# Kernel tuning notes

Measured on AMD Instinct MI355X. Metric: run time of the kernel, lower is better.

## Reference

```python
import jax, jax.numpy as jnp
import numpy as np

V = 32000   # vocab
T = 256     # context len
C = 384     # n_embed
H = 6       # heads
D = 64      # head dim (HEAD_SIZE // NUM_HEADS)
L = 6       # blocks
B = 16      # batch
FF = 4 * C


def setup_inputs() -> dict:
    key = jax.random.key(0)
    ks = jax.random.split(key, 16)
    s = 0.02
    p = {}
    p["x_ids"] = jax.random.randint(ks[0], (B, T), 0, V)
    p["y_ids"] = jax.random.randint(ks[1], (B, T), 0, V)
    p["tok_emb"] = jax.random.normal(ks[2], (V, C), jnp.float32) * s
    p["pos_emb"] = jax.random.normal(ks[3], (T, C), jnp.float32) * s
    p["Wq"] = jax.random.normal(ks[4], (L, H, C, D), jnp.float32) * s
    p["Wk"] = jax.random.normal(ks[5], (L, H, C, D), jnp.float32) * s
    p["Wv"] = jax.random.normal(ks[6], (L, H, C, D), jnp.float32) * s
    p["Wo"] = jax.random.normal(ks[7], (L, H * D, C), jnp.float32) * s
    p["bo"] = jnp.zeros((L, C), jnp.float32)
    p["ln1_s"] = jnp.ones((L, C), jnp.float32)
    p["ln1_b"] = jnp.zeros((L, C), jnp.float32)
    p["ln2_s"] = jnp.ones((L, C), jnp.float32)
    p["ln2_b"] = jnp.zeros((L, C), jnp.float32)
    p["W1"] = jax.random.normal(ks[8], (L, C, FF), jnp.float32) * s
    p["b1"] = jnp.zeros((L, FF), jnp.float32)
    p["W2"] = jax.random.normal(ks[9], (L, FF, C), jnp.float32) * s
    p["b2"] = jnp.zeros((L, C), jnp.float32)
    p["lnf_s"] = jnp.ones((C,), jnp.float32)
    p["lnf_b"] = jnp.zeros((C,), jnp.float32)
    p["Whead"] = jax.random.normal(ks[10], (C, V), jnp.float32) * s
    p["bhead"] = jnp.zeros((V,), jnp.float32)
    return p


def _ln(x, scale, bias, eps=1e-5):
    m = x.mean(-1, keepdims=True)
    v = ((x - m) ** 2).mean(-1, keepdims=True)
    return (x - m) * jax.lax.rsqrt(v + eps) * scale + bias


def reference(x_ids, y_ids, tok_emb, pos_emb, Wq, Wk, Wv, Wo, bo,
              ln1_s, ln1_b, ln2_s, ln2_b, W1, b1, W2, b2,
              lnf_s, lnf_b, Whead, bhead):
    Bq, Tq = x_ids.shape
    x = tok_emb[x_ids] + pos_emb[:Tq]                      # [B,T,C]
    mask = jnp.tril(jnp.ones((Tq, Tq), bool))
    scale = C ** -0.5  # NOTE: original scales by input dim C, not head dim
    for l in range(L):
        h = _ln(x, ln1_s[l], ln1_b[l])
        q = jnp.einsum('btc,hcd->bhtd', h, Wq[l])
        k = jnp.einsum('btc,hcd->bhtd', h, Wk[l])
        v = jnp.einsum('btc,hcd->bhtd', h, Wv[l])
        att = jnp.einsum('bhtd,bhsd->bhts', q, k) * scale
        att = jnp.where(mask, att, -jnp.inf)
        att = jax.nn.softmax(att, axis=-1)
        o = jnp.einsum('bhts,bhsd->bhtd', att, v)
        o = o.transpose(0, 2, 1, 3).reshape(Bq, Tq, H * D)  # concat heads
        x = x + o @ Wo[l] + bo[l]
        h2 = _ln(x, ln2_s[l], ln2_b[l])
        x = x + jax.nn.relu(h2 @ W1[l] + b1[l]) @ W2[l] + b2[l]
    x = _ln(x, lnf_s, lnf_b)
    logits = x @ Whead + bhead                             # [B,T,V]
    logp = jax.nn.log_softmax(logits, axis=-1)
    loss = -jnp.take_along_axis(logp, y_ids[..., None], axis=-1).mean()
    return (logits, loss)
```

## Files before the change

### kernel.cpp

```cpp
#include <hip/hip_runtime.h>

typedef unsigned short u16;
typedef u16   u16x8 __attribute__((ext_vector_type(8)));
typedef short s16x8 __attribute__((ext_vector_type(8)));
typedef float f32x4 __attribute__((ext_vector_type(4)));

#define NV 32000
#define NT 256
#define NC 384
#define NH 6
#define ND 64
#define NL 6
#define NB 16
#define NFF 1536
#define NM (NB*NT)
#define QKVSZ (NB*NH*NT*ND)
#define NSLAB (NV/128)

__device__ __forceinline__ u16 f2bf(float f){
    unsigned x = __builtin_bit_cast(unsigned, f);
    x += 0x7fffu + ((x>>16)&1u);
    return (u16)(x>>16);
}

__device__ __forceinline__ void gload_lds16(const u16* g, u16* l){
    __builtin_amdgcn_global_load_lds((const __attribute__((address_space(1))) unsigned int*)g,
                                     (__attribute__((address_space(3))) unsigned int*)l, 16, 0, 0);
}

__global__ __launch_bounds__(256) void embed_ln(const int* __restrict__ ids,
        const float* __restrict__ tok, const float* __restrict__ pos,
        const float* __restrict__ sc, const float* __restrict__ bi,
        float* __restrict__ x, u16* __restrict__ out){
    int row  = blockIdx.x*4 + (threadIdx.x>>6);
    int lane = threadIdx.x & 63;
    int t = row & (NT-1);
    const float* tr = tok + (size_t)ids[row]*NC;
    const float* pr = pos + (size_t)t*NC;
    float* xr = x + (size_t)row*NC;
    float v[6]; float sum = 0.f, sq = 0.f;
    #pragma unroll
    for (int i=0;i<6;++i){
        int c = lane+64*i;
        v[i] = tr[c] + pr[c];
        xr[c] = v[i];
        sum += v[i]; sq += v[i]*v[i];
    }
    #pragma unroll
    for (int off=1; off<64; off<<=1){ sum += __shfl_xor(sum,off); sq += __shfl_xor(sq,off); }
    float mean = sum*(1.f/NC);
    float rstd = rsqrtf(sq*(1.f/NC) - mean*mean + 1e-5f);
    u16* orow = out + (size_t)row*NC;
    #pragma unroll
    for (int i=0;i<6;++i){ int c = lane+64*i; orow[c] = f2bf((v[i]-mean)*rstd*sc[c] + bi[c]); }
}

__global__ __launch_bounds__(256) void ln_kernel(const float* __restrict__ x,
        const float* __restrict__ sc, const float* __restrict__ bi, u16* __restrict__ out){
    int row  = blockIdx.x*4 + (threadIdx.x>>6);
    int lane = threadIdx.x & 63;
    const float* xr = x + (size_t)row*NC;
    float v[6]; float sum = 0.f, sq = 0.f;
    #pragma unroll
    for (int i=0;i<6;++i){ v[i]=xr[lane+64*i]; sum+=v[i]; sq+=v[i]*v[i]; }
    #pragma unroll
    for (int off=1; off<64; off<<=1){ sum += __shfl_xor(sum,off); sq += __shfl_xor(sq,off); }
    float mean = sum*(1.f/NC);
    float rstd = rsqrtf(sq*(1.f/NC) - mean*mean + 1e-5f);
    u16* orow = out + (size_t)row*NC;
    #pragma unroll
    for (int i=0;i<6;++i){ int c = lane+64*i; orow[c] = f2bf((v[i]-mean)*rstd*sc[c] + bi[c]); }
}

struct TDesc {
    const float* in; u16* out;
    int Cc; int nx; int perZ; int obDiv; int oStride; int start;
    long inBatch; long oS1; long oS2; float scale;
};
struct TPack { TDesc d[7]; };

__global__ __launch_bounds__(256) void tconv_all(TPack p){
    __shared__ float tile[32][33];
    int bid = blockIdx.x;
    int e = 0;
    #pragma unroll
    for (int i=1;i<7;++i) e += (bid >= p.d[i].start) ? 1 : 0;
    TDesc D = p.d[e];
    int local = bid - D.start;
    int bz  = local / D.perZ; int rem = local - bz*D.perZ;
    int cy  = rem / D.nx;     int cx  = rem - cy*D.nx;
    int r0 = cy*32, c0 = cx*32;
    const float* ib = D.in + (size_t)bz*D.inBatch;
    u16* ob = D.out + (size_t)(bz/D.obDiv)*D.oS1 + (size_t)(bz%D.obDiv)*D.oS2;
    int tx = threadIdx.x & 31, ty = threadIdx.x >> 5;
    #pragma unroll
    for (int i=0;i<4;++i) tile[ty+8*i][tx] = ib[(size_t)(r0+ty+8*i)*D.Cc + (c0+tx)];
    __syncthreads();
    #pragma unroll
    for (int i=0;i<4;++i) ob[(size_t)(c0+ty+8*i)*D.oStride + (r0+tx)] = f2bf(tile[tx][ty+8*i]*D.scale);
}

template<int EPI, int BM, int BN, int SWZ>
__global__ __launch_bounds__(256,2) void gemm_bt(
        const u16* __restrict__ A, const u16* __restrict__ Bt,
        const float* __restrict__ bias, float* __restrict__ resid,
        u16* __restrict__ outb, float* __restrict__ outf, float* __restrict__ lpart,
        int M, int N, int K){
    constexpr int WM = BM/2, WN = BN/2, MI = WM/16, NI = WN/16;
    __shared__ u16 As[2*BM*32];
    __shared__ u16 Bs[2*BN*32];
    int tid = threadIdx.x;
    int lane = tid & 63, wid = tid >> 6;
    int wm = wid >> 1, wn = wid & 1;
    int l15 = lane & 15, lg = lane >> 4;
    int bx, by;
    if (SWZ){
        int nwg = gridDim.x*gridDim.y;
        int orig = blockIdx.y*gridDim.x + blockIdx.x;
        int swz = (orig&7)*(nwg>>3) + (orig>>3);
        by = swz & 31;
        bx = swz >> 5;
    } else { bx = blockIdx.x; by = blockIdx.y; }
    int m0 = by * BM, n0 = bx * BN;
    f32x4 acc[MI][NI];
    #pragma unroll
    for (int a=0;a<MI;++a)
        #pragma unroll
        for (int b=0;b<NI;++b) acc[a][b] = f32x4{0.f,0.f,0.f,0.f};

    int nk = K >> 6;
    for (int kk = 0; kk < nk; ++kk){
        int k0 = kk << 6;
        #pragma unroll
        for (int h=0;h<2;++h){
            #pragma unroll
            for (int i=0;i<BM/64;++i){
                int o   = i*4096 + tid*16;
                int row = o >> 6;
                int kb  = (o & 63) >> 1;
                gload_lds16(A + (size_t)(m0+row)*K + (k0+h*32+kb), As + h*BM*32 + (o>>1));
            }
            #pragma unroll
            for (int i=0;i<BN/64;++i){
                int o   = i*4096 + tid*16;
                int row = o >> 6;
                int kb  = (o & 63) >> 1;
                gload_lds16(Bt + (size_t)(n0+row)*K + (k0+h*32+kb), Bs + h*BN*32 + (o>>1));
            }
        }
        asm volatile("s_waitcnt vmcnt(0)" ::: "memory");
        __syncthreads();
        #pragma unroll
        for (int ks=0;ks<2;++ks){
            s16x8 af[MI], bfr[NI];
            #pragma unroll
            for (int mi=0;mi<MI;++mi) af[mi]  = *(const s16x8*)&As[ks*BM*32 + (wm*WM+mi*16+l15)*32 + lg*8];
            #pragma unroll
            for (int ni=0;ni<NI;++ni) bfr[ni] = *(const s16x8*)&Bs[ks*BN*32 + (wn*WN+ni*16+l15)*32 + lg*8];
            #pragma unroll
            for (int mi=0;mi<MI;++mi)
                #pragma unroll
                for (int ni=0;ni<NI;++ni)
                    acc[mi][ni] = __builtin_amdgcn_mfma_f32_16x16x32_bf16(af[mi], bfr[ni], acc[mi][ni], 0,0,0);
        }
        __syncthreads();
    }

    if (EPI == 3){
        float es[MI][4];
        #pragma unroll
        for (int mi=0;mi<MI;++mi)
            #pragma unroll
            for (int r=0;r<4;++r) es[mi][r] = 0.f;
        #pragma unroll
        for (int mi=0;mi<MI;++mi)
            #pragma unroll
            for (int ni=0;ni<NI;++ni)
                #pragma unroll
                for (int r=0;r<4;++r){
                    int mg = m0 + wm*WM + mi*16 + lg*4 + r;
                    int ng = n0 + wn*WN + ni*16 + l15;
                    float val = acc[mi][ni][r] + bias[ng];
                    outf[(size_t)mg*N + ng] = val;
                    es[mi][r] += __expf(val);
                }
        #pragma unroll
        for (int mi=0;mi<MI;++mi)
            #pragma unroll
            for (int r=0;r<4;++r){
                float s = es[mi][r];
                s += __shfl_xor(s,1); s += __shfl_xor(s,2);
                s += __shfl_xor(s,4); s += __shfl_xor(s,8);
                if (l15 == 0){
                    int mg = m0 + wm*WM + mi*16 + lg*4 + r;
                    lpart[(size_t)mg*NSLAB + bx*2 + wn] = s;
                }
            }
        return;
    }

    #pragma unroll
    for (int mi=0;mi<MI;++mi){
        #pragma unroll
        for (int ni=0;ni<NI;++ni){
            #pragma unroll
            for (int r=0;r<4;++r){
                int mg = m0 + wm*WM + mi*16 + lg*4 + r;
                int ng = n0 + wn*WN + ni*16 + l15;
                float c = acc[mi][ni][r];
                if (EPI == 0){
                    int which = ng / NC; int hd = ng - which*NC;
                    int hh = hd >> 6, d = hd & 63;
                    int bb = mg >> 8, tt = mg & (NT-1);
                    outb[(size_t)which*QKVSZ + ((size_t)(bb*NH+hh)*NT + tt)*ND + d] = f2bf(c);
                } else if (EPI == 1){
                    float* pp = resid + (size_t)mg*N + ng;
                    *pp = *pp + c + bias[ng];
                } else if (EPI == 2){
                    outb[(size_t)mg*N + ng] = f2bf(fmaxf(c + bias[ng], 0.f));
                }
            }
        }
    }
}

__global__ __launch_bounds__(256,2) void attn_kernel(const u16* __restrict__ qkv, u16* __restrict__ o){
    int blk = blockIdx.x;
    int qt = blk & 3, bh = blk >> 2;
    int b = bh / NH, h = bh - b*NH;
    int tid = threadIdx.x, lane = tid & 63, w = tid >> 6;
    int l15 = lane & 15, lg = lane >> 4;
    __shared__ u16 Ks[256*72];
    __shared__ u16 Vt[64*264];
    __shared__ u16 Ps[4][16*72];
    const u16* qb = qkv + (size_t)bh*NT*ND;
    const u16* kb = qb + QKVSZ;
    const u16* vb = kb + QKVSZ;
    int nit = (qt+1)*2;
    for (int it=0; it<nit; ++it){
        int idx = it*256 + tid;
        int e0 = idx*8;
        int row = e0 >> 6, col = e0 & 63;
        *(u16x8*)&Ks[row*72+col] = *(const u16x8*)(kb + e0);
        u16x8 vv = *(const u16x8*)(vb + e0);
        #pragma unroll
        for (int j=0;j<8;++j) Vt[(col+j)*264 + row] = vv[j];
    }
    const u16* qrow = qb + (size_t)(qt*64 + w*16 + l15)*ND;
    s16x8 qf[2];
    qf[0] = *(const s16x8*)(qrow + lg*8);
    qf[1] = *(const s16x8*)(qrow + 32 + lg*8);
    __syncthreads();

    f32x4 oacc[4]; float l_[4];
    #pragma unroll
    for (int c=0;c<4;++c){ oacc[c]=f32x4{0.f,0.f,0.f,0.f}; l_[c]=0.f; }
    u16* Pw = &Ps[w][0];

    for (int kt=0; kt<=qt; ++kt){
        f32x4 sacc[4];
        #pragma unroll
        for (int c=0;c<4;++c) sacc[c]=f32x4{0.f,0.f,0.f,0.f};
        #pragma unroll
        for (int ks=0;ks<2;++ks){
            s16x8 kf[4];
            #pragma unroll
            for (int ni=0;ni<4;++ni)
                kf[ni] = *(const s16x8*)&Ks[(kt*64+ni*16+l15)*72 + ks*32 + lg*8];
            #pragma unroll
            for (int ni=0;ni<4;++ni)
                sacc[ni] = __builtin_amdgcn_mfma_f32_16x16x32_bf16(qf[ks], kf[ni], sacc[ni], 0,0,0);
        }
        if (kt == qt){
            #pragma unroll
            for (int ni=0;ni<4;++ni)
                #pragma unroll
                for (int r=0;r<4;++r)
                    if (ni*16+l15 > w*16+lg*4+r) sacc[ni][r] = -1e30f;
        }
        #pragma unroll
        for (int r=0;r<4;++r){
            float rs = 0.f;
            #pragma unroll
            for (int ni=0;ni<4;++ni){
                float p = __expf(sacc[ni][r]);
                sacc[ni][r] = p;
                rs += p;
                Pw[(lg*4+r)*72 + ni*16 + l15] = f2bf(p);
            }
            rs += __shfl_xor(rs,1); rs += __shfl_xor(rs,2);
            rs += __shfl_xor(rs,4); rs += __shfl_xor(rs,8);
            l_[r] += rs;
        }
        #pragma unroll
        for (int ks=0;ks<2;++ks){
            s16x8 pf, vf[4];
            pf = *(const s16x8*)&Pw[l15*72 + ks*32 + lg*8];
            #pragma unroll
            for (int ni=0;ni<4;++ni)
                vf[ni] = *(const s16x8*)&Vt[(ni*16+l15)*264 + kt*64 + ks*32 + lg*8];
            #pragma unroll
            for (int ni=0;ni<4;++ni)
                oacc[ni] = __builtin_amdgcn_mfma_f32_16x16x32_bf16(pf, vf[ni], oacc[ni], 0,0,0);
        }
    }
    #pragma unroll
    for (int ni=0;ni<4;++ni)
        #pragma unroll
        for (int r=0;r<4;++r){
            int t = qt*64 + w*16 + lg*4 + r;
            int d = ni*16 + l15;
            o[((size_t)(b*NT + t))*NC + h*ND + d] = f2bf(oacc[ni][r] / l_[r]);
        }
}

__global__ __launch_bounds__(256) void loss_rows2(const float* __restrict__ lpart,
        const float* __restrict__ logits, const int* __restrict__ y, float* __restrict__ rowloss){
    int row  = blockIdx.x*4 + (threadIdx.x>>6);
    int lane = threadIdx.x & 63;
    const float* pr = lpart + (size_t)row*NSLAB;
    float s = 0.f;
    for (int i = lane; i < NSLAB; i += 64) s += pr[i];
    #pragma unroll
    for (int off=1; off<64; off<<=1) s += __shfl_xor(s, off);
    if (lane==0)
        rowloss[row] = logf(s) - logits[(size_t)row*NV + y[row]];
}

__global__ __launch_bounds__(256) void loss_final(const float* __restrict__ rowloss, float* __restrict__ out){
    int tid = threadIdx.x;
    float s = 0.f;
    for (int i = tid; i < NM; i += 256) s += rowloss[i];
    #pragma unroll
    for (int off=1; off<64; off<<=1) s += __shfl_xor(s, off);
    __shared__ float ss[4];
    if ((tid&63)==0) ss[tid>>6]=s;
    __syncthreads();
    if (tid==0) out[0] = (ss[0]+ss[1]+ss[2]+ss[3]) * (1.f/NM);
}

extern "C" void kernel_launch(void* const* d_in, const int* in_sizes, int n_in,
                              void* d_out, int out_size, void* d_ws, size_t ws_size,
                              hipStream_t stream){
    const int*   x_ids = (const int*)  d_in[0];
    const int*   y_ids = (const int*)  d_in[1];
    const float* tok   = (const float*)d_in[2];
    const float* pos   = (const float*)d_in[3];
    const float* Wq    = (const float*)d_in[4];
    const float* Wk    = (const float*)d_in[5];
    const float* Wv    = (const float*)d_in[6];
    const float* Wo    = (const float*)d_in[7];
    const float* bo    = (const float*)d_in[8];
    const float* ln1s  = (const float*)d_in[9];
    const float* ln1b  = (const float*)d_in[10];
    const float* ln2s  = (const float*)d_in[11];
    const float* ln2b  = (const float*)d_in[12];
    const float* W1    = (const float*)d_in[13];
    const float* b1    = (const float*)d_in[14];
    const float* W2    = (const float*)d_in[15];
    const float* b2    = (const float*)d_in[16];
    const float* lnfs  = (const float*)d_in[17];
    const float* lnfb  = (const float*)d_in[18];
    const float* Wh    = (const float*)d_in[19];
    const float* bh    = (const float*)d_in[20];

    float* logits = (float*)d_out;
    float* lossp  = logits + (size_t)NM*NV;

    char* ws = (char*)d_ws;
    auto alloc = [&](size_t bytes)->char*{ char* p = ws; ws += (bytes + 255) & ~(size_t)255; return p; };
    float* xf    = (float*)alloc((size_t)NM*NC*4);
    u16*   hbf   = (u16*)  alloc((size_t)NM*NC*2);
    u16*   qkvb  = (u16*)  alloc((size_t)3*QKVSZ*2);
    u16*   obf   = (u16*)  alloc((size_t)NM*NC*2);
    u16*   f1bf  = (u16*)  alloc((size_t)NM*NFF*2);
    u16*   qkvw  = (u16*)  alloc((size_t)NL*1152*NC*2);
    u16*   wot   = (u16*)  alloc((size_t)NL*NC*NC*2);
    u16*   w1t   = (u16*)  alloc((size_t)NL*NFF*NC*2);
    u16*   w2t   = (u16*)  alloc((size_t)NL*NC*NFF*2);
    u16*   wht   = (u16*)  alloc((size_t)NV*NC*2);
    float* part  = (float*)alloc((size_t)NM*4);
    float* lpart = (float*)qkvb;

    const float qscale = 0.051031036307982884f;

    TPack tp;
    tp.d[0] = {Wq, qkvw + 0*(NC*NC), ND,  2,  24, NH, NC, 0,     (long)NC*ND, (long)1152*NC, (long)ND*NC, qscale};
    tp.d[1] = {Wk, qkvw + 1*(NC*NC), ND,  2,  24, NH, NC, 864,   (long)NC*ND, (long)1152*NC, (long)ND*NC, 1.f};
    tp.d[2] = {Wv, qkvw + 2*(NC*NC), ND,  2,  24, NH, NC, 1728,  (long)NC*ND, (long)1152*NC, (long)ND*NC, 1.f};
    tp.d[3] = {Wo, wot,              NC, 12, 144, 1,  NC, 2592,  (long)NC*NC, (long)NC*NC,   0,           1.f};
    tp.d[4] = {W1, w1t,             NFF, 48, 576, 1,  NC, 3456,  (long)NC*NFF,(long)NFF*NC,  0,           1.f};
    tp.d[5] = {W2, w2t,              NC, 12, 576, 1, NFF, 6912,  (long)NFF*NC,(long)NC*NFF,  0,           1.f};
    tp.d[6] = {Wh, wht,              NV,1000,12000,1, NC, 10368, 0,           0,             0,           1.f};
    tconv_all<<<22368,256,0,stream>>>(tp);

    embed_ln<<<NM/4,256,0,stream>>>(x_ids, tok, pos, ln1s, ln1b, xf, hbf);
    for (int l = 0; l < NL; ++l){
        gemm_bt<0,64,128,0><<<dim3(1152/128, NM/64),256,0,stream>>>(hbf, qkvw + (size_t)l*1152*NC,
                nullptr, nullptr, qkvb, nullptr, nullptr, NM, 1152, NC);
        attn_kernel<<<NB*NH*4,256,0,stream>>>(qkvb, obf);
        gemm_bt<1,64,128,0><<<dim3(NC/128, NM/64),256,0,stream>>>(obf, wot + (size_t)l*NC*NC,
                bo + l*NC, xf, nullptr, nullptr, nullptr, NM, NC, NC);
        ln_kernel<<<NM/4,256,0,stream>>>(xf, ln2s + l*NC, ln2b + l*NC, hbf);
        gemm_bt<2,64,128,0><<<dim3(NFF/128, NM/64),256,0,stream>>>(hbf, w1t + (size_t)l*NFF*NC,
                b1 + l*NFF, nullptr, f1bf, nullptr, nullptr, NM, NFF, NC);
        gemm_bt<1,64,128,0><<<dim3(NC/128, NM/64),256,0,stream>>>(f1bf, w2t + (size_t)l*NC*NFF,
                b2 + l*NC, xf, nullptr, nullptr, nullptr, NM, NC, NFF);
        if (l < NL-1)
            ln_kernel<<<NM/4,256,0,stream>>>(xf, ln1s + (l+1)*NC, ln1b + (l+1)*NC, hbf);
        else
            ln_kernel<<<NM/4,256,0,stream>>>(xf, lnfs, lnfb, hbf);
    }
    gemm_bt<3,128,256,1><<<dim3(NV/256, NM/128),256,0,stream>>>(hbf, wht, bh,
            nullptr, nullptr, logits, lpart, NM, NV, NC);
    loss_rows2<<<NM/4,256,0,stream>>>(lpart, logits, y_ids, part);
    loss_final<<<1,256,0,stream>>>(part, lossp);
}
```

Measured before the change: 850.6 us.

## Double-buffer GEMM LDS tiles and shrink LM-head tile to 128x128

Converts the bf16 GEMM main loop to a two-stage LDS double buffer: the next K-tile is issued with global_load_lds before computing the current one, and a partial vmcnt wait replaces the full drain. This lets global memory latency overlap with MFMA work. The LM-head GEMM also moves from a 128x256 to a 128x128 tile, which doubles its grid and the per-row partial-slab count (NSLAB). Doubled LDS use may reduce occupancy. The vmcnt(L) wait count has to match the number of loads issued per stage.

```diff
diff --git a/kernel.cpp b/kernel.cpp
--- a/kernel.cpp
+++ b/kernel.cpp
@@ -15,7 +15,7 @@
 #define NFF 1536
 #define NM (NB*NT)
 #define QKVSZ (NB*NH*NT*ND)
-#define NSLAB (NV/128)
+#define NSLAB (NV/64)
 
 __device__ __forceinline__ u16 f2bf(float f){
     unsigned x = __builtin_bit_cast(unsigned, f);
@@ -26,6 +26,18 @@
 __device__ __forceinline__ void gload_lds16(const u16* g, u16* l){
     __builtin_amdgcn_global_load_lds((const __attribute__((address_space(1))) unsigned int*)g,
                                      (__attribute__((address_space(3))) unsigned int*)l, 16, 0, 0);
+}
+
+template<int N> __device__ __forceinline__ void wait_vm(){
+    static_assert(N==0 || N==6 || N==8, "add literal");
+    if constexpr (N==0) asm volatile("s_waitcnt vmcnt(0)" ::: "memory");
+    if constexpr (N==6) asm volatile("s_waitcnt vmcnt(6)" ::: "memory");
+    if constexpr (N==8) asm volatile("s_waitcnt vmcnt(8)" ::: "memory");
+}
+__device__ __forceinline__ void bar(){
+    asm volatile("" ::: "memory");
+    __builtin_amdgcn_s_barrier();
+    asm volatile("" ::: "memory");
 }
 
 __global__ __launch_bounds__(256) void embed_ln(const int* __restrict__ ids,
@@ -107,8 +119,9 @@
         u16* __restrict__ outb, float* __restrict__ outf, float* __restrict__ lpart,
         int M, int N, int K){
     constexpr int WM = BM/2, WN = BN/2, MI = WM/16, NI = WN/16;
-    __shared__ u16 As[2*BM*32];
-    __shared__ u16 Bs[2*BN*32];
+    constexpr int L = (BM+BN)/32;
+    __shared__ u16 As[2][2*BM*32];
+    __shared__ u16 Bs[2][2*BN*32];
     int tid = threadIdx.x;
     int lane = tid & 63, wid = tid >> 6;
     int wm = wid >> 1, wn = wid & 1;
@@ -128,9 +141,8 @@
         #pragma unroll
         for (int b=0;b<NI;++b) acc[a][b] = f32x4{0.f,0.f,0.f,0.f};
 
-    int nk = K >> 6;
-    for (int kk = 0; kk < nk; ++kk){
-        int k0 = kk << 6;
+    auto STAGE = [&](int kt, int buf){
+        int k0 = kt << 6;
         #pragma unroll
         for (int h=0;h<2;++h){
             #pragma unroll
@@ -138,32 +150,39 @@
                 int o   = i*4096 + tid*16;
                 int row = o >> 6;
                 int kb  = (o & 63) >> 1;
-                gload_lds16(A + (size_t)(m0+row)*K + (k0+h*32+kb), As + h*BM*32 + (o>>1));
+                gload_lds16(A + (size_t)(m0+row)*K + (k0+h*32+kb), &As[buf][h*BM*32 + (o>>1)]);
             }
             #pragma unroll
             for (int i=0;i<BN/64;++i){
                 int o   = i*4096 + tid*16;
                 int row = o >> 6;
                 int kb  = (o & 63) >> 1;
-                gload_lds16(Bt + (size_t)(n0+row)*K + (k0+h*32+kb), Bs + h*BN*32 + (o>>1));
+                gload_lds16(Bt + (size_t)(n0+row)*K + (k0+h*32+kb), &Bs[buf][h*BN*32 + (o>>1)]);
             }
         }
-        asm volatile("s_waitcnt vmcnt(0)" ::: "memory");
-        __syncthreads();
+    };
+
+    int nk = K >> 6;
+    STAGE(0, 0);
+    for (int t = 0; t < nk; ++t){
+        int buf = t & 1;
+        if (t+1 < nk){ STAGE(t+1, buf^1); wait_vm<L>(); }
+        else         { wait_vm<0>(); }
+        bar();
         #pragma unroll
         for (int ks=0;ks<2;++ks){
             s16x8 af[MI], bfr[NI];
             #pragma unroll
-            for (int mi=0;mi<MI;++mi) af[mi]  = *(const s16x8*)&As[ks*BM*32 + (wm*WM+mi*16+l15)*32 + lg*8];
-            #pragma unroll
-            for (int ni=0;ni<NI;++ni) bfr[ni] = *(const s16x8*)&Bs[ks*BN*32 + (wn*WN+ni*16+l15)*32 + lg*8];
+            for (int mi=0;mi<MI;++mi) af[mi]  = *(const s16x8*)&As[buf][ks*BM*32 + (wm*WM+mi*16+l15)*32 + lg*8];
+            #pragma unroll
+            for (int ni=0;ni<NI;++ni) bfr[ni] = *(const s16x8*)&Bs[buf][ks*BN*32 + (wn*WN+ni*16+l15)*32 + lg*8];
             #pragma unroll
             for (int mi=0;mi<MI;++mi)
                 #pragma unroll
                 for (int ni=0;ni<NI;++ni)
                     acc[mi][ni] = __builtin_amdgcn_mfma_f32_16x16x32_bf16(af[mi], bfr[ni], acc[mi][ni], 0,0,0);
         }
-        __syncthreads();
+        bar();
     }
 
     if (EPI == 3){
@@ -411,7 +430,7 @@
         else
             ln_kernel<<<NM/4,256,0,stream>>>(xf, lnfs, lnfb, hbf);
     }
-    gemm_bt<3,128,256,1><<<dim3(NV/256, NM/128),256,0,stream>>>(hbf, wht, bh,
+    gemm_bt<3,128,128,1><<<dim3(NV/128, NM/128),256,0,stream>>>(hbf, wht, bh,
             nullptr, nullptr, logits, lpart, NM, NV, NC);
     loss_rows2<<<NM/4,256,0,stream>>>(lpart, logits, y_ids, part);
     loss_final<<<1,256,0,stream>>>(part, lossp);
```

Measured after the change: 886.9 us. +4.3%, slower.

## Fuse residual add and LayerNorm into full-row projection GEMM epilogues

Applied to the files above, without the earlier changes.

Adds a GEMM epilogue for the Wo and W2 projections. It covers a full 384-column row per block (32x384 tiles), adds bias and residual, and computes the next LayerNorm with a cross-wave shared-memory reduction. This removes the separate ln_kernel launches and their extra pass over the residual stream. The GEMM also gains a BK template parameter and reorders fragment loads, and the LM-head GEMM moves to 128x128 tiles with finer loss partial slabs. The fused GEMMs launch only 128 blocks, with one block streaming the whole weight matrix per row strip, so parallelism drops.

```diff
diff --git a/kernel.cpp b/kernel.cpp
--- a/kernel.cpp
+++ b/kernel.cpp
@@ -15,7 +15,7 @@
 #define NFF 1536
 #define NM (NB*NT)
 #define QKVSZ (NB*NH*NT*ND)
-#define NSLAB (NV/128)
+#define NSLAB (NV/64)
 
 __device__ __forceinline__ u16 f2bf(float f){
     unsigned x = __builtin_bit_cast(unsigned, f);
@@ -55,23 +55,6 @@
     for (int i=0;i<6;++i){ int c = lane+64*i; orow[c] = f2bf((v[i]-mean)*rstd*sc[c] + bi[c]); }
 }
 
-__global__ __launch_bounds__(256) void ln_kernel(const float* __restrict__ x,
-        const float* __restrict__ sc, const float* __restrict__ bi, u16* __restrict__ out){
-    int row  = blockIdx.x*4 + (threadIdx.x>>6);
-    int lane = threadIdx.x & 63;
-    const float* xr = x + (size_t)row*NC;
-    float v[6]; float sum = 0.f, sq = 0.f;
-    #pragma unroll
-    for (int i=0;i<6;++i){ v[i]=xr[lane+64*i]; sum+=v[i]; sq+=v[i]*v[i]; }
-    #pragma unroll
-    for (int off=1; off<64; off<<=1){ sum += __shfl_xor(sum,off); sq += __shfl_xor(sq,off); }
-    float mean = sum*(1.f/NC);
-    float rstd = rsqrtf(sq*(1.f/NC) - mean*mean + 1e-5f);
-    u16* orow = out + (size_t)row*NC;
-    #pragma unroll
-    for (int i=0;i<6;++i){ int c = lane+64*i; orow[c] = f2bf((v[i]-mean)*rstd*sc[c] + bi[c]); }
-}
-
 struct TDesc {
     const float* in; u16* out;
     int Cc; int nx; int perZ; int obDiv; int oStride; int start;
@@ -100,15 +83,16 @@
     for (int i=0;i<4;++i) ob[(size_t)(c0+ty+8*i)*D.oStride + (r0+tx)] = f2bf(tile[tx][ty+8*i]*D.scale);
 }
 
-template<int EPI, int BM, int BN, int SWZ>
+template<int EPI, int BM, int BN, int BK, int SWZ>
 __global__ __launch_bounds__(256,2) void gemm_bt(
         const u16* __restrict__ A, const u16* __restrict__ Bt,
         const float* __restrict__ bias, float* __restrict__ resid,
         u16* __restrict__ outb, float* __restrict__ outf, float* __restrict__ lpart,
+        const float* __restrict__ lnsc, const float* __restrict__ lnbi,
         int M, int N, int K){
-    constexpr int WM = BM/2, WN = BN/2, MI = WM/16, NI = WN/16;
-    __shared__ u16 As[2*BM*32];
-    __shared__ u16 Bs[2*BN*32];
+    constexpr int WM = BM/2, WN = BN/2, MI = WM/16, NI = WN/16, KH = BK/32;
+    __shared__ u16 As[KH*BM*32];
+    __shared__ u16 Bs[KH*BN*32];
     int tid = threadIdx.x;
     int lane = tid & 63, wid = tid >> 6;
     int wm = wid >> 1, wn = wid & 1;
@@ -128,40 +112,49 @@
         #pragma unroll
         for (int b=0;b<NI;++b) acc[a][b] = f32x4{0.f,0.f,0.f,0.f};
 
-    int nk = K >> 6;
+    int nk = K / BK;
     for (int kk = 0; kk < nk; ++kk){
-        int k0 = kk << 6;
-        #pragma unroll
-        for (int h=0;h<2;++h){
-            #pragma unroll
-            for (int i=0;i<BM/64;++i){
-                int o   = i*4096 + tid*16;
-                int row = o >> 6;
-                int kb  = (o & 63) >> 1;
-                gload_lds16(A + (size_t)(m0+row)*K + (k0+h*32+kb), As + h*BM*32 + (o>>1));
+        int k0 = kk * BK;
+        #pragma unroll
+        for (int h=0;h<KH;++h){
+            if constexpr (BM >= 64){
+                #pragma unroll
+                for (int i=0;i<BM/64;++i){
+                    int o   = i*4096 + tid*16;
+                    int row = o >> 6;
+                    int kb  = (o & 63) >> 1;
+                    gload_lds16(A + (size_t)(m0+row)*K + (k0+h*32+kb), &As[h*BM*32 + (o>>1)]);
+                }
+            } else {
+                if (tid < BM*4){
+                    int o = tid*16;
+                    int row = o >> 6;
+                    int kb  = (o & 63) >> 1;
+                    gload_lds16(A + (size_t)(m0+row)*K + (k0+h*32+kb), &As[h*BM*32 + (o>>1)]);
+                }
             }
             #pragma unroll
             for (int i=0;i<BN/64;++i){
                 int o   = i*4096 + tid*16;
                 int row = o >> 6;
                 int kb  = (o & 63) >> 1;
-                gload_lds16(Bt + (size_t)(n0+row)*K + (k0+h*32+kb), Bs + h*BN*32 + (o>>1));
+                gload_lds16(Bt + (size_t)(n0+row)*K + (k0+h*32+kb), &Bs[h*BN*32 + (o>>1)]);
             }
         }
         asm volatile("s_waitcnt vmcnt(0)" ::: "memory");
         __syncthreads();
         #pragma unroll
-        for (int ks=0;ks<2;++ks){
-            s16x8 af[MI], bfr[NI];
-            #pragma unroll
-            for (int mi=0;mi<MI;++mi) af[mi]  = *(const s16x8*)&As[ks*BM*32 + (wm*WM+mi*16+l15)*32 + lg*8];
-            #pragma unroll
-            for (int ni=0;ni<NI;++ni) bfr[ni] = *(const s16x8*)&Bs[ks*BN*32 + (wn*WN+ni*16+l15)*32 + lg*8];
-            #pragma unroll
-            for (int mi=0;mi<MI;++mi)
+        for (int ks=0;ks<KH;++ks){
+            s16x8 af[MI];
+            #pragma unroll
+            for (int mi=0;mi<MI;++mi) af[mi] = *(const s16x8*)&As[ks*BM*32 + (wm*WM+mi*16+l15)*32 + lg*8];
+            #pragma unroll
+            for (int ni=0;ni<NI;++ni){
+                s16x8 bfr = *(const s16x8*)&Bs[ks*BN*32 + (wn*WN+ni*16+l15)*32 + lg*8];
                 #pragma unroll
-                for (int ni=0;ni<NI;++ni)
-                    acc[mi][ni] = __builtin_amdgcn_mfma_f32_16x16x32_bf16(af[mi], bfr[ni], acc[mi][ni], 0,0,0);
+                for (int mi=0;mi<MI;++mi)
+                    acc[mi][ni] = __builtin_amdgcn_mfma_f32_16x16x32_bf16(af[mi], bfr, acc[mi][ni], 0,0,0);
+            }
         }
         __syncthreads();
     }
@@ -199,6 +192,47 @@
         return;
     }
 
+    if (EPI == 4){
+        __shared__ float redS[2][16][2];
+        __shared__ float redQ[2][16][2];
+        float rowS[4] = {0.f,0.f,0.f,0.f}, rowQ[4] = {0.f,0.f,0.f,0.f};
+        #pragma unroll
+        for (int ni=0;ni<NI;++ni)
+            #pragma unroll
+            for (int r=0;r<4;++r){
+                int mg = m0 + wm*WM + lg*4 + r;
+                int ng = wn*WN + ni*16 + l15;
+                float val = acc[0][ni][r] + bias[ng] + resid[(size_t)mg*NC + ng];
+                resid[(size_t)mg*NC + ng] = val;
+                acc[0][ni][r] = val;
+                rowS[r] += val; rowQ[r] += val*val;
+            }
+        #pragma unroll
+        for (int r=0;r<4;++r){
+            rowS[r] += __shfl_xor(rowS[r],1); rowQ[r] += __shfl_xor(rowQ[r],1);
+            rowS[r] += __shfl_xor(rowS[r],2); rowQ[r] += __shfl_xor(rowQ[r],2);
+            rowS[r] += __shfl_xor(rowS[r],4); rowQ[r] += __shfl_xor(rowQ[r],4);
+            rowS[r] += __shfl_xor(rowS[r],8); rowQ[r] += __shfl_xor(rowQ[r],8);
+            if (l15 == 0){ redS[wm][lg*4+r][wn] = rowS[r]; redQ[wm][lg*4+r][wn] = rowQ[r]; }
+        }
+        __syncthreads();
+        #pragma unroll
+        for (int r=0;r<4;++r){
+            int rr = lg*4 + r;
+            float S = redS[wm][rr][0] + redS[wm][rr][1];
+            float Q = redQ[wm][rr][0] + redQ[wm][rr][1];
+            float mean = S*(1.f/NC);
+            float rstd = rsqrtf(Q*(1.f/NC) - mean*mean + 1e-5f);
+            int mg = m0 + wm*WM + rr;
+            #pragma unroll
+            for (int ni=0;ni<NI;++ni){
+                int ng = wn*WN + ni*16 + l15;
+                outb[(size_t)mg*NC + ng] = f2bf((acc[0][ni][r]-mean)*rstd*lnsc[ng] + lnbi[ng]);
+            }
+        }
+        return;
+    }
+
     #pragma unroll
     for (int mi=0;mi<MI;++mi){
         #pragma unroll
@@ -213,9 +247,6 @@
                     int hh = hd >> 6, d = hd & 63;
                     int bb = mg >> 8, tt = mg & (NT-1);
                     outb[(size_t)which*QKVSZ + ((size_t)(bb*NH+hh)*NT + tt)*ND + d] = f2bf(c);
-                } else if (EPI == 1){
-                    float* pp = resid + (size_t)mg*N + ng;
-                    *pp = *pp + c + bias[ng];
                 } else if (EPI == 2){
                     outb[(size_t)mg*N + ng] = f2bf(fmaxf(c + bias[ng], 0.f));
                 }
@@ -396,23 +427,20 @@
 
     embed_ln<<<NM/4,256,0,stream>>>(x_ids, tok, pos, ln1s, ln1b, xf, hbf);
     for (int l = 0; l < NL; ++l){
-        gemm_bt<0,64,128,0><<<dim3(1152/128, NM/64),256,0,stream>>>(hbf, qkvw + (size_t)l*1152*NC,
-                nullptr, nullptr, qkvb, nullptr, nullptr, NM, 1152, NC);
+        gemm_bt<0,64,128,64,0><<<dim3(1152/128, NM/64),256,0,stream>>>(hbf, qkvw + (size_t)l*1152*NC,
+                nullptr, nullptr, qkvb, nullptr, nullptr, nullptr, nullptr, NM, 1152, NC);
         attn_kernel<<<NB*NH*4,256,0,stream>>>(qkvb, obf);
-        gemm_bt<1,64,128,0><<<dim3(NC/128, NM/64),256,0,stream>>>(obf, wot + (size_t)l*NC*NC,
-                bo + l*NC, xf, nullptr, nullptr, nullptr, NM, NC, NC);
-        ln_kernel<<<NM/4,256,0,stream>>>(xf, ln2s + l*NC, ln2b + l*NC, hbf);
-        gemm_bt<2,64,128,0><<<dim3(NFF/128, NM/64),256,0,stream>>>(hbf, w1t + (size_t)l*NFF*NC,
-                b1 + l*NFF, nullptr, f1bf, nullptr, nullptr, NM, NFF, NC);
-        gemm_bt<1,64,128,0><<<dim3(NC/128, NM/64),256,0,stream>>>(f1bf, w2t + (size_t)l*NC*NFF,
-                b2 + l*NC, xf, nullptr, nullptr, nullptr, NM, NC, NFF);
-        if (l < NL-1)
-            ln_kernel<<<NM/4,256,0,stream>>>(xf, ln1s + (l+1)*NC, ln1b + (l+1)*NC, hbf);
-        else
-            ln_kernel<<<NM/4,256,0,stream>>>(xf, lnfs, lnfb, hbf);
-    }
-    gemm_bt<3,128,256,1><<<dim3(NV/256, NM/128),256,0,stream>>>(hbf, wht, bh,
-            nullptr, nullptr, logits, lpart, NM, NV, NC);
+        gemm_bt<4,32,384,32,0><<<dim3(1, NM/32),256,0,stream>>>(obf, wot + (size_t)l*NC*NC,
+                bo + l*NC, xf, hbf, nullptr, nullptr, ln2s + l*NC, ln2b + l*NC, NM, NC, NC);
+        gemm_bt<2,64,128,64,0><<<dim3(NFF/128, NM/64),256,0,stream>>>(hbf, w1t + (size_t)l*NFF*NC,
+                b1 + l*NFF, nullptr, f1bf, nullptr, nullptr, nullptr, nullptr, NM, NFF, NC);
+        const float* nsc = (l < NL-1) ? (ln1s + (l+1)*NC) : lnfs;
+        const float* nbi = (l < NL-1) ? (ln1b + (l+1)*NC) : lnfb;
+        gemm_bt<4,32,384,32,0><<<dim3(1, NM/32),256,0,stream>>>(f1bf, w2t + (size_t)l*NC*NFF,
+                b2 + l*NC, xf, hbf, nullptr, nullptr, nsc, nbi, NM, NC, NFF);
+    }
+    gemm_bt<3,128,128,64,1><<<dim3(NV/128, NM/128),256,0,stream>>>(hbf, wht, bh,
+            nullptr, nullptr, logits, lpart, nullptr, nullptr, NM, NV, NC);
     loss_rows2<<<NM/4,256,0,stream>>>(lpart, logits, y_ids, part);
     loss_final<<<1,256,0,stream>>>(part, lossp);
 }
```

New measurement: 998.2 us. +17.4%, slower.
